# Optimization experiments

Measured on AMD Instinct MI355X. Metric: run time of the kernel, lower is better.

## Reference

```python
import jax, jax.numpy as jnp
import numpy as np

N = 10000
E = 80000
NUM_TYPES = 1000
IN_CH = 64
EMB = 128
IN_GNN = EMB + IN_CH - 1  # 191
NUM_GRAPHS = 16
NUM_CLASSES = 2


def _glorot(key, shape):
    fan_in, fan_out = shape[0], shape[1]
    lim = jnp.sqrt(6.0 / (fan_in + fan_out))
    return jax.random.uniform(key, shape, jnp.float32, -lim, lim)


def setup_inputs() -> dict:
    key = jax.random.key(0)
    ks = jax.random.split(key, 20)
    node_type_ids = jax.random.randint(ks[0], (N,), 0, NUM_TYPES)
    other_feats = jax.random.normal(ks[1], (N, IN_CH - 1), jnp.float32)
    edge_index = jax.random.randint(ks[2], (2, E), 0, N)
    batch = jnp.sort(jax.random.randint(ks[3], (N,), 0, NUM_GRAPHS))
    params = dict(
        emb=jax.random.normal(ks[4], (NUM_TYPES, EMB), jnp.float32),
        W1=_glorot(ks[5], (IN_GNN, 2048)), b1=jnp.zeros((2048,), jnp.float32),
        W2=_glorot(ks[6], (2048, 1024)), b2=jnp.zeros((1024,), jnp.float32),
        W3=_glorot(ks[7], (1024, 1024)), b3=jnp.zeros((1024,), jnp.float32),
        h1w=_glorot(ks[8], (1024, 1024)), h1b=jnp.zeros((1024,), jnp.float32),
        h2w=_glorot(ks[9], (1024, 1024)), h2b=jnp.zeros((1024,), jnp.float32),
        h3w=_glorot(ks[10], (1024, 512)), h3b=jnp.zeros((512,), jnp.float32),
        ow=_glorot(ks[11], (512, NUM_CLASSES)), ob=jnp.zeros((NUM_CLASSES,), jnp.float32),
    )
    return dict(node_type_ids=node_type_ids, other_feats=other_feats,
                edge_index=edge_index, batch=batch, **params)


def _gcn_norm(edge_index, num_nodes):
    # add self loops + symmetric normalization D^-1/2 (A+I) D^-1/2 (PyG GCNConv defaults)
    loop = jnp.arange(num_nodes, dtype=edge_index.dtype)
    src = jnp.concatenate([edge_index[0], loop])
    dst = jnp.concatenate([edge_index[1], loop])
    deg = jax.ops.segment_sum(jnp.ones_like(src, jnp.float32), dst, num_segments=num_nodes)
    dinv = jnp.where(deg > 0, jax.lax.rsqrt(jnp.maximum(deg, 1.0)), 0.0)
    norm = dinv[src] * dinv[dst]
    return src, dst, norm


def _gcn_conv(x, src, dst, norm, W, b):
    h = x @ W                                    # [N, out] dense GEMM first (PyG order)
    msg = h[src] * norm[:, None]                 # gather + scale over edges
    agg = jax.ops.segment_sum(msg, dst, num_segments=x.shape[0])  # scatter-add
    return agg + b


def reference(node_type_ids, other_feats, edge_index, batch,
              emb, W1, b1, W2, b2, W3, b3,
              h1w, h1b, h2w, h2b, h3w, h3b, ow, ob):
    # eval mode: dropout is identity
    x = jnp.concatenate([emb[node_type_ids], other_feats], axis=-1)  # [N, 191]
    src, dst, norm = _gcn_norm(edge_index, x.shape[0])
    x = jax.nn.relu(_gcn_conv(x, src, dst, norm, W1, b1))
    x = jax.nn.relu(_gcn_conv(x, src, dst, norm, W2, b2))
    x = jax.nn.relu(_gcn_conv(x, src, dst, norm, W3, b3))
    # global mean pool over graphs
    sums = jax.ops.segment_sum(x, batch, num_segments=NUM_GRAPHS)
    cnts = jax.ops.segment_sum(jnp.ones((x.shape[0],), jnp.float32), batch, num_segments=NUM_GRAPHS)
    g = sums / jnp.maximum(cnts, 1.0)[:, None]   # [G, 1024]
    g = jax.nn.relu(g @ h1w + h1b)
    g = jax.nn.relu(g @ h2w + h2b)
    g = jax.nn.relu(g @ h3w + h3b)
    return g @ ow + ob                           # [G, num_classes]
```

## Files before the change

### kernel.cpp

```cpp
#include <hip/hip_runtime.h>


#define N_NODES 10000
#define N_EDGES 80000
#define EMB_DIM 128
#define FEAT_DIM 63
#define IN_GNN 191
#define IN_STRIDE 192
#define H1 2048
#define H2 1024
#define NGRAPH 16
#define NCLS 2
#define PCHUNK 8

using ushort = unsigned short;
typedef __attribute__((ext_vector_type(8))) short s8b;
typedef __attribute__((ext_vector_type(4))) float f4v;

__device__ __forceinline__ float us2f(ushort u) {
    union { unsigned int i; float f; } v; v.i = ((unsigned int)u) << 16; return v.f;
}
__device__ __forceinline__ ushort f2us(float f) {
    union { unsigned int i; float f; } v; v.f = f;
    unsigned int r = v.i + 0x7FFFu + ((v.i >> 16) & 1u);
    return (ushort)(r >> 16);
}
__device__ __forceinline__ float ldm(const void* p, long i, int md) {
    return (md == 1) ? us2f(((const ushort*)p)[i]) : ((const float*)p)[i];
}

__global__ void GraphV1EmbLarge_73864847556672_kernel() {}

__global__ void k_detect(const ushort* __restrict__ feats, int* __restrict__ mode) {
    if (threadIdx.x != 0 || blockIdx.x != 0) return;
    int sane = 0;
    for (int i = 0; i < 256; i++) {
        ushort u = feats[i];
        int e = (u >> 7) & 0xFF;
        if (u == 0 || (e >= 97 && e <= 157)) sane++;
    }
    *mode = (sane >= 220) ? 1 : 2;
}

__global__ void k_zero2(int* __restrict__ a, int na, float* __restrict__ b, int nb) {
    int i = blockIdx.x * 256 + threadIdx.x;
    if (i < na) a[i] = 0;
    if (i < nb) b[i] = 0.f;
}
__global__ void k_deg_i(const int* __restrict__ dst, int* __restrict__ cnt) {
    int e = blockIdx.x * blockDim.x + threadIdx.x;
    if (e < N_EDGES) atomicAdd(&cnt[dst[e]], 1);
}
__global__ void k_scan(const int* __restrict__ cnt, int* __restrict__ indptr,
                       float* __restrict__ dinv) {
    __shared__ int part[256];
    int t = threadIdx.x;
    int base = t * 40;
    int s = 0;
    for (int i = 0; i < 40; i++) { int idx = base + i; if (idx < N_NODES) s += cnt[idx]; }
    part[t] = s;
    __syncthreads();
    if (t == 0) {
        int run = 0;
        for (int i = 0; i < 256; i++) { int tmp = part[i]; part[i] = run; run += tmp; }
        indptr[N_NODES] = run;
    }
    __syncthreads();
    int run = part[t];
    for (int i = 0; i < 40; i++) {
        int idx = base + i;
        if (idx < N_NODES) {
            indptr[idx] = run; run += cnt[idx];
            dinv[idx] = rsqrtf((float)cnt[idx] + 1.0f);
        }
    }
}
__global__ void k_fill(const int* __restrict__ src, const int* __restrict__ dst,
                       const int* __restrict__ indptr, int* __restrict__ cursor,
                       const float* __restrict__ dinv, int* __restrict__ ecol,
                       float* __restrict__ ewgt) {
    int e = blockIdx.x * blockDim.x + threadIdx.x;
    if (e >= N_EDGES) return;
    int d = dst[e], s = src[e];
    int slot = indptr[d] + atomicAdd(&cursor[d], 1);
    ecol[slot] = s;
    ewgt[slot] = dinv[s] * dinv[d];
}
__global__ void k_starts(const int* __restrict__ batch, int* __restrict__ starts) {
    int i = blockIdx.x * blockDim.x + threadIdx.x;
    if (i > N_NODES) return;
    int bc = (i < N_NODES) ? batch[i] : NGRAPH;
    int bp = (i == 0) ? -1 : batch[i - 1];
    for (int g = bp + 1; g <= bc; g++) starts[g] = i;
}

__global__ void k_build_x0(const int* __restrict__ types, const void* __restrict__ emb,
                           const void* __restrict__ feats, ushort* __restrict__ x0,
                           const int* __restrict__ mode) {
    int md = *mode;
    int i = blockIdx.x;
    int c = threadIdx.x;
    float v = 0.f;
    if (c < EMB_DIM) v = ldm(emb, (long)types[i] * EMB_DIM + c, md);
    else if (c < IN_GNN) v = ldm(feats, (long)i * FEAT_DIM + (c - EMB_DIM), md);
    x0[(long)i * IN_STRIDE + c] = f2us(v);
}

__device__ __forceinline__ void cvt_tile(const void* W, int K, int N, int Kp,
                                         ushort* Wt, int n0, int k0, int md) {
    __shared__ float tile[32][33];
    int tx = threadIdx.x, ty = threadIdx.y;
    for (int r = ty; r < 32; r += 8) {
        int k = k0 + r;
        tile[r][tx] = (k < K) ? ldm(W, (long)k * N + n0 + tx, md) : 0.f;
    }
    __syncthreads();
    for (int r = ty; r < 32; r += 8) {
        int nn = n0 + r, kk = k0 + tx;
        if (kk < Kp) Wt[(long)nn * Kp + kk] = f2us(tile[tx][r]);
    }
}

__global__ void k_cvtT_all(const void* W1, const void* W2, const void* W3,
                           const void* h1, const void* h2, const void* h3,
                           ushort* W1t, ushort* W2t, ushort* W3t,
                           ushort* h1t, ushort* h2t, ushort* h3t,
                           const int* __restrict__ mode) {
    int md = *mode;
    int b = blockIdx.x;
    if (b < 384) {
        int t = b;        cvt_tile(W1, IN_GNN, H1, IN_STRIDE, W1t, (t % 64) * 32, (t / 64) * 32, md);
    } else if (b < 2432) {
        int t = b - 384;  cvt_tile(W2, H1, H2, H1, W2t, (t % 32) * 32, (t / 32) * 32, md);
    } else if (b < 3456) {
        int t = b - 2432; cvt_tile(W3, H2, H2, H2, W3t, (t % 32) * 32, (t / 32) * 32, md);
    } else if (b < 4480) {
        int t = b - 3456; cvt_tile(h1, H2, H2, H2, h1t, (t % 32) * 32, (t / 32) * 32, md);
    } else if (b < 5504) {
        int t = b - 4480; cvt_tile(h2, H2, H2, H2, h2t, (t % 32) * 32, (t / 32) * 32, md);
    } else {
        int t = b - 5504; cvt_tile(h3, H2, 512, H2, h3t, (t % 16) * 32, (t / 16) * 32, md);
    }
}

__global__ void k_biases(const void* __restrict__ b1, const void* __restrict__ b2,
                         const void* __restrict__ b3, float* __restrict__ b1f,
                         float* __restrict__ b2f, float* __restrict__ b3f,
                         const int* __restrict__ mode) {
    int md = *mode;
    int i = blockIdx.x * 256 + threadIdx.x;
    if (i < 2048) b1f[i] = ldm(b1, i, md);
    else if (i < 3072) b2f[i - 2048] = ldm(b2, (long)(i - 2048), md);
    else if (i < 4096) b3f[i - 3072] = ldm(b3, (long)(i - 3072), md);
}

__global__ void k_gather192(const ushort* __restrict__ H, const int* __restrict__ indptr,
                            const int* __restrict__ ecol, const float* __restrict__ ewgt,
                            const float* __restrict__ dinv, ushort* __restrict__ X) {
    int d = blockIdx.x;
    int c = threadIdx.x;
    float ds = dinv[d];
    float acc = us2f(H[(long)d * IN_STRIDE + c]) * ds * ds;
    int s0 = indptr[d], s1 = indptr[d + 1];
    for (int s = s0; s < s1; s++) {
        int sc = ecol[s];
        float w = ewgt[s];
        acc += us2f(H[(long)sc * IN_STRIDE + c]) * w;
    }
    X[(long)d * IN_STRIDE + c] = f2us(acc);
}

__device__ __forceinline__ void unpack8(uint4 u, float* f) {
    f[0] = us2f((ushort)(u.x & 0xffff)); f[1] = us2f((ushort)(u.x >> 16));
    f[2] = us2f((ushort)(u.y & 0xffff)); f[3] = us2f((ushort)(u.y >> 16));
    f[4] = us2f((ushort)(u.z & 0xffff)); f[5] = us2f((ushort)(u.z >> 16));
    f[6] = us2f((ushort)(u.w & 0xffff)); f[7] = us2f((ushort)(u.w >> 16));
}

__global__ void k_gather1024(const ushort* __restrict__ H, const int* __restrict__ indptr,
                             const int* __restrict__ ecol, const float* __restrict__ ewgt,
                             const float* __restrict__ dinv, const float* __restrict__ bias,
                             ushort* __restrict__ X) {
    int d = blockIdx.x;
    int c8 = threadIdx.x * 8;
    float ds = dinv[d];
    float a[8], f[8];
    unpack8(*(const uint4*)&H[(long)d * H2 + c8], a);
    float w0 = ds * ds;
#pragma unroll
    for (int r = 0; r < 8; r++) a[r] *= w0;
    int s0 = indptr[d], s1 = indptr[d + 1];
    for (int s = s0; s < s1; s++) {
        int sc = ecol[s];
        float w = ewgt[s];
        unpack8(*(const uint4*)&H[(long)sc * H2 + c8], f);
#pragma unroll
        for (int r = 0; r < 8; r++) a[r] += f[r] * w;
    }
    uint4 o;
    unsigned int p0 = (unsigned int)f2us(fmaxf(a[0] + bias[c8 + 0], 0.f));
    unsigned int p1 = (unsigned int)f2us(fmaxf(a[1] + bias[c8 + 1], 0.f));
    unsigned int p2 = (unsigned int)f2us(fmaxf(a[2] + bias[c8 + 2], 0.f));
    unsigned int p3 = (unsigned int)f2us(fmaxf(a[3] + bias[c8 + 3], 0.f));
    unsigned int p4 = (unsigned int)f2us(fmaxf(a[4] + bias[c8 + 4], 0.f));
    unsigned int p5 = (unsigned int)f2us(fmaxf(a[5] + bias[c8 + 5], 0.f));
    unsigned int p6 = (unsigned int)f2us(fmaxf(a[6] + bias[c8 + 6], 0.f));
    unsigned int p7 = (unsigned int)f2us(fmaxf(a[7] + bias[c8 + 7], 0.f));
    o.x = p0 | (p1 << 16); o.y = p2 | (p3 << 16);
    o.z = p4 | (p5 << 16); o.w = p6 | (p7 << 16);
    *(uint4*)&X[(long)d * H2 + c8] = o;
}

__global__ __launch_bounds__(256) void k_mfma_gemm(
    const ushort* __restrict__ A, int lda, int M,
    const ushort* __restrict__ Wt, int K, int N,
    const float* __restrict__ bias, int relu,
    ushort* __restrict__ C, int NB) {
    __shared__ ushort As[128 * 32];
    __shared__ ushort Bs[128 * 32];
    int L = blockIdx.x;
    int i = L >> 3;
    int m_t = (L & 7) + (i / NB) * 8;
    int n_t = i % NB;
    int m0 = m_t * 128, n0 = n_t * 128;
    if (m0 >= M) return;
    int tid = threadIdx.x;
    int wave = tid >> 6, lane = tid & 63;
    int wm = (wave & 1) * 64, wn = (wave >> 1) * 64;
    int quad = lane >> 4, l16 = lane & 15;
    int srow = tid >> 2;
    int scol = (tid & 3) * 8;
    int swz = ((srow >> 1) & 3) << 3;
    int rwz = ((l16 >> 1) & 3) << 3;
    int wa0 = srow * 32 + (scol ^ swz);
    int wa1 = (64 + srow) * 32 + (scol ^ swz);

    f4v acc[4][4];
#pragma unroll
    for (int ii = 0; ii < 4; ii++)
#pragma unroll
        for (int jj = 0; jj < 4; jj++) acc[ii][jj] = (f4v)(0.f);

    int gm1 = m0 + srow;       if (gm1 >= M) gm1 = M - 1;
    int gm2 = m0 + 64 + srow;  if (gm2 >= M) gm2 = M - 1;
    const ushort* pa1 = A + (long)gm1 * lda + scol;
    const ushort* pa2 = A + (long)gm2 * lda + scol;
    const ushort* pb1 = Wt + (long)(n0 + srow) * K + scol;
    const ushort* pb2 = Wt + (long)(n0 + 64 + srow) * K + scol;

    s8b va1 = *(const s8b*)pa1;
    s8b va2 = *(const s8b*)pa2;
    s8b vb1 = *(const s8b*)pb1;
    s8b vb2 = *(const s8b*)pb2;

    for (int k0 = 0; k0 < K; k0 += 32) {
        __syncthreads();
        *(s8b*)&As[wa0] = va1;
        *(s8b*)&As[wa1] = va2;
        *(s8b*)&Bs[wa0] = vb1;
        *(s8b*)&Bs[wa1] = vb2;
        __syncthreads();
        if (k0 + 32 < K) {
            pa1 += 32; pa2 += 32; pb1 += 32; pb2 += 32;
            va1 = *(const s8b*)pa1;
            va2 = *(const s8b*)pa2;
            vb1 = *(const s8b*)pb1;
            vb2 = *(const s8b*)pb2;
        }
        s8b a[4], b[4];
#pragma unroll
        for (int ii = 0; ii < 4; ii++)
            a[ii] = *(const s8b*)&As[(wm + ii * 16 + l16) * 32 + (quad * 8 ^ rwz)];
#pragma unroll
        for (int jj = 0; jj < 4; jj++)
            b[jj] = *(const s8b*)&Bs[(wn + jj * 16 + l16) * 32 + (quad * 8 ^ rwz)];
#pragma unroll
        for (int ii = 0; ii < 4; ii++)
#pragma unroll
            for (int jj = 0; jj < 4; jj++)
                acc[ii][jj] = __builtin_amdgcn_mfma_f32_16x16x32_bf16(a[ii], b[jj], acc[ii][jj], 0, 0, 0);
    }

#pragma unroll
    for (int ii = 0; ii < 4; ii++) {
        int row0 = m0 + wm + ii * 16 + quad * 4;
#pragma unroll
        for (int jj = 0; jj < 4; jj++) {
            int colc = n0 + wn + jj * 16 + l16;
            float bv = bias ? bias[colc] : 0.f;
#pragma unroll
            for (int r = 0; r < 4; r++) {
                int row = row0 + r;
                if (row < M) {
                    float v = acc[ii][jj][r] + bv;
                    if (relu) v = fmaxf(v, 0.f);
                    C[(long)row * N + colc] = f2us(v);
                }
            }
        }
    }
}

__global__ void k_pool_part(const ushort* __restrict__ x, const int* __restrict__ starts,
                            float* __restrict__ acc) {
    int g = blockIdx.x / PCHUNK, ch = blockIdx.x % PCHUNK;
    int c = blockIdx.y * 256 + threadIdx.x;
    int s0 = starts[g], s1 = starts[g + 1];
    int len = s1 - s0;
    int per = (len + PCHUNK - 1) / PCHUNK;
    int r0 = s0 + ch * per;
    int r1 = r0 + per; if (r1 > s1) r1 = s1;
    if (r0 >= r1) return;
    float sum = 0.f;
    for (int i = r0; i < r1; i++) sum += us2f(x[(long)i * H2 + c]);
    atomicAdd(&acc[g * H2 + c], sum);
}
__global__ void k_pool_fin(const float* __restrict__ acc, const int* __restrict__ starts,
                           ushort* __restrict__ pA) {
    int idx = blockIdx.x * 256 + threadIdx.x;
    if (idx >= NGRAPH * H2) return;
    int g = idx >> 10;
    int cnt = starts[g + 1] - starts[g];
    pA[idx] = f2us(acc[idx] / (float)(cnt > 0 ? cnt : 1));
}

__global__ __launch_bounds__(256) void k_head_mfma(const ushort* __restrict__ A,
                                                   const ushort* __restrict__ Wt,
                                                   float* __restrict__ pt, int N) {
    __shared__ float red[4][16][16];
    int n0 = blockIdx.x * 16;
    int ks = blockIdx.y;
    int wave = threadIdx.x >> 6, lane = threadIdx.x & 63;
    int l16 = lane & 15, quad = lane >> 4;
    int kbase = ks * 256 + wave * 64;
    f4v acc = (f4v)(0.f);
#pragma unroll
    for (int kk = 0; kk < 64; kk += 32) {
        int k = kbase + kk + quad * 8;
        s8b a = *(const s8b*)&A[l16 * 1024 + k];
        s8b b = *(const s8b*)&Wt[(long)(n0 + l16) * 1024 + k];
        acc = __builtin_amdgcn_mfma_f32_16x16x32_bf16(a, b, acc, 0, 0, 0);
    }
#pragma unroll
    for (int r = 0; r < 4; r++) red[wave][quad * 4 + r][l16] = acc[r];
    __syncthreads();
    int row = threadIdx.x >> 4, col = threadIdx.x & 15;
    float s = red[0][row][col] + red[1][row][col] + red[2][row][col] + red[3][row][col];
    pt[((long)ks * 16 + row) * N + n0 + col] = s;
}

__global__ void k_head_red(const float* __restrict__ pt, const void* __restrict__ bias,
                           ushort* __restrict__ out, int N,
                           const int* __restrict__ mode) {
    int md = *mode;
    int idx = blockIdx.x * 256 + threadIdx.x;
    if (idx >= 16 * N) return;
    int row = idx / N, col = idx - row * N;
    float s = pt[((long)0 * 16 + row) * N + col] + pt[((long)1 * 16 + row) * N + col]
            + pt[((long)2 * 16 + row) * N + col] + pt[((long)3 * 16 + row) * N + col];
    s = fmaxf(s + ldm(bias, (long)col, md), 0.f);
    out[(long)row * N + col] = f2us(s);
}

__global__ void k_head_out(const ushort* __restrict__ in, const void* __restrict__ W,
                           const void* __restrict__ b, void* __restrict__ out,
                           const int* __restrict__ mode) {
    int md = *mode;
    int row = blockIdx.x >> 1, cls = blockIdx.x & 1;
    int lane = threadIdx.x;
    float acc = 0.f;
    for (int k = lane; k < 512; k += 64)
        acc += us2f(in[row * 512 + k]) * ldm(W, (long)k * NCLS + cls, md);
#pragma unroll
    for (int off = 32; off > 0; off >>= 1) acc += __shfl_down(acc, off);
    if (lane == 0) {
        float v = acc + ldm(b, (long)cls, md);
        if (md == 1) ((ushort*)out)[row * NCLS + cls] = f2us(v);
        else ((float*)out)[row * NCLS + cls] = v;
    }
}

extern "C" void kernel_launch(void* const* d_in, const int* in_sizes, int n_in,
                              void* d_out, int out_size, void* d_ws, size_t ws_size,
                              hipStream_t stream) {
    static const int EXPECT[19] = {
        10000, 630000, 160000, 10000, 128000,
        391168, 2048, 2097152, 1024, 1048576, 1024,
        1048576, 1024, 1048576, 1024, 524288, 512, 1024, 2
    };
    if (n_in != 19) { hipMemsetAsync(d_out, 0x48, 64, stream); return; }
    for (int i = 0; i < 19; i++)
        if (in_sizes[i] != EXPECT[i]) { hipMemsetAsync(d_out, 0x50 + i, 64, stream); return; }
    if (ws_size < (size_t)90000000) { hipMemsetAsync(d_out, 0x49, 64, stream); return; }

    const int* node_types = (const int*)d_in[0];
    const void* other = d_in[1];
    const int* e_src = (const int*)d_in[2];
    const int* e_dst = e_src + N_EDGES;
    const int* batch = (const int*)d_in[3];

    char* w = (char*)d_ws;
    int* mode = (int*)w;      w += 256;
    int* cnt = (int*)w;       w += 10240 * 4;
    int* cursor = (int*)w;    w += 10240 * 4;
    float* dinv = (float*)w;  w += 10240 * 4;
    int* starts = (int*)w;    w += 256;
    int* indptr = (int*)w;    w += 10240 * 4;
    int* ecol = (int*)w;      w += 81920 * 4;
    float* ewgt = (float*)w;  w += 81920 * 4;
    float* b1f = (float*)w;   w += 2048 * 4;
    float* b2f = (float*)w;   w += 1024 * 4;
    float* b3f = (float*)w;   w += 1024 * 4;
    float* pt = (float*)w;    w += 4 * 16 * 1024 * 4;
    float* pacc = (float*)w;  w += 16 * 1024 * 4;
    ushort* pA = (ushort*)w;  w += 16 * 1024 * 2;
    ushort* hA = (ushort*)w;  w += 16 * 1024 * 2;
    ushort* hB = (ushort*)w;  w += 16 * 1024 * 2;
    ushort* x0 = (ushort*)w;  w += 1920000 * 2;
    ushort* A1 = (ushort*)w;  w += 1920000 * 2;
    ushort* W1t = (ushort*)w; w += 393216 * 2;
    ushort* W2t = (ushort*)w; w += 2097152 * 2;
    ushort* W3t = (ushort*)w; w += 1048576 * 2;
    ushort* h1wt = (ushort*)w; w += 1048576 * 2;
    ushort* h2wt = (ushort*)w; w += 1048576 * 2;
    ushort* h3wt = (ushort*)w; w += 524288 * 2;
    ushort* Hb = (ushort*)w;  w += 20480000 * 2;
    ushort* Gb = (ushort*)w;  w += 10240000 * 2;
    ushort* x2 = Hb;
    ushort* x3 = Hb + (size_t)N_NODES * H2;

    hipGetLastError();
    k_detect<<<1, 64, 0, stream>>>((const ushort*)other, mode);
    hipError_t e0 = hipGetLastError();
    if (e0 != hipSuccess) { hipMemsetAsync(d_out, 0x46, 64, stream); return; }

    k_zero2<<<80, 256, 0, stream>>>(cnt, 20480, pacc, NGRAPH * H2);
    k_deg_i<<<(N_EDGES + 255) / 256, 256, 0, stream>>>(e_dst, cnt);
    k_starts<<<(N_NODES + 256) / 256, 256, 0, stream>>>(batch, starts);
    k_scan<<<1, 256, 0, stream>>>(cnt, indptr, dinv);
    k_fill<<<(N_EDGES + 255) / 256, 256, 0, stream>>>(e_src, e_dst, indptr, cursor, dinv, ecol, ewgt);

    k_build_x0<<<N_NODES, IN_STRIDE, 0, stream>>>(node_types, d_in[4], other, x0, mode);
    k_cvtT_all<<<6016, dim3(32, 8), 0, stream>>>(d_in[5], d_in[7], d_in[9], d_in[11], d_in[13], d_in[15],
                                                 W1t, W2t, W3t, h1wt, h2wt, h3wt, mode);
    k_biases<<<16, 256, 0, stream>>>(d_in[6], d_in[8], d_in[10], b1f, b2f, b3f, mode);

    k_gather192<<<N_NODES, IN_STRIDE, 0, stream>>>(x0, indptr, ecol, ewgt, dinv, A1);
    k_mfma_gemm<<<16 * 80, 256, 0, stream>>>(A1, IN_STRIDE, N_NODES, W1t, IN_STRIDE, H1, b1f, 1, Hb, 16);

    k_mfma_gemm<<<8 * 80, 256, 0, stream>>>(Hb, H1, N_NODES, W2t, H1, H2, nullptr, 0, Gb, 8);
    k_gather1024<<<N_NODES, 128, 0, stream>>>(Gb, indptr, ecol, ewgt, dinv, b2f, x2);

    k_mfma_gemm<<<8 * 80, 256, 0, stream>>>(x2, H2, N_NODES, W3t, H2, H2, nullptr, 0, Gb, 8);
    k_gather1024<<<N_NODES, 128, 0, stream>>>(Gb, indptr, ecol, ewgt, dinv, b3f, x3);

    k_pool_part<<<dim3(NGRAPH * PCHUNK, H2 / 256), 256, 0, stream>>>(x3, starts, pacc);
    k_pool_fin<<<64, 256, 0, stream>>>(pacc, starts, pA);

    k_head_mfma<<<dim3(64, 4), 256, 0, stream>>>(pA, h1wt, pt, 1024);
    k_head_red<<<64, 256, 0, stream>>>(pt, d_in[12], hA, 1024, mode);
    k_head_mfma<<<dim3(64, 4), 256, 0, stream>>>(hA, h2wt, pt, 1024);
    k_head_red<<<64, 256, 0, stream>>>(pt, d_in[14], hB, 1024, mode);
    k_head_mfma<<<dim3(32, 4), 256, 0, stream>>>(hB, h3wt, pt, 512);
    k_head_red<<<32, 256, 0, stream>>>(pt, d_in[16], hA, 512, mode);
    k_head_out<<<NGRAPH * NCLS, 64, 0, stream>>>(hA, d_in[17], d_in[18], d_out, mode);

    hipError_t e1 = hipGetLastError();
    if (e1 != hipSuccess) hipMemsetAsync(d_out, 0x47, 64, stream);
}
```

Baseline: 408.9 us.

## Double-buffer GEMM shared tiles and unroll sparse gather loops by two

The bf16 MFMA GEMM now uses two LDS buffers for the A and B tiles. The next K-slice is written into the alternate buffer while the current one is consumed, which drops one __syncthreads per K iteration. Separately, both CSR gather kernels process two neighbor edges per loop iteration so two row loads are in flight together, raising memory-level parallelism. The cost is doubled LDS use in the GEMM, which may reduce occupancy, plus slightly higher register pressure in the gathers.

After: 403.1 us. Within noise of the previous version (-1.4%).

```diff
diff --git a/kernel.cpp b/kernel.cpp
--- a/kernel.cpp
+++ b/kernel.cpp
@@ -162,11 +162,15 @@
     float ds = dinv[d];
     float acc = us2f(H[(long)d * IN_STRIDE + c]) * ds * ds;
     int s0 = indptr[d], s1 = indptr[d + 1];
-    for (int s = s0; s < s1; s++) {
-        int sc = ecol[s];
-        float w = ewgt[s];
-        acc += us2f(H[(long)sc * IN_STRIDE + c]) * w;
-    }
+    int s = s0;
+    for (; s + 1 < s1; s += 2) {
+        int sa = ecol[s], sb = ecol[s + 1];
+        float wa = ewgt[s], wb = ewgt[s + 1];
+        float fa = us2f(H[(long)sa * IN_STRIDE + c]);
+        float fb = us2f(H[(long)sb * IN_STRIDE + c]);
+        acc += fa * wa + fb * wb;
+    }
+    if (s < s1) acc += us2f(H[(long)ecol[s] * IN_STRIDE + c]) * ewgt[s];
     X[(long)d * IN_STRIDE + c] = f2us(acc);
 }
 
@@ -184,18 +188,29 @@
     int d = blockIdx.x;
     int c8 = threadIdx.x * 8;
     float ds = dinv[d];
-    float a[8], f[8];
+    float a[8], f0[8], f1[8];
     unpack8(*(const uint4*)&H[(long)d * H2 + c8], a);
     float w0 = ds * ds;
 #pragma unroll
     for (int r = 0; r < 8; r++) a[r] *= w0;
     int s0 = indptr[d], s1 = indptr[d + 1];
-    for (int s = s0; s < s1; s++) {
-        int sc = ecol[s];
-        float w = ewgt[s];
-        unpack8(*(const uint4*)&H[(long)sc * H2 + c8], f);
-#pragma unroll
-        for (int r = 0; r < 8; r++) a[r] += f[r] * w;
+    int s = s0;
+    for (; s + 1 < s1; s += 2) {
+        int sa = ecol[s], sb = ecol[s + 1];
+        float wa = ewgt[s], wb = ewgt[s + 1];
+        uint4 ua = *(const uint4*)&H[(long)sa * H2 + c8];
+        uint4 ub = *(const uint4*)&H[(long)sb * H2 + c8];
+        unpack8(ua, f0);
+        unpack8(ub, f1);
+#pragma unroll
+        for (int r = 0; r < 8; r++) a[r] += f0[r] * wa + f1[r] * wb;
+    }
+    if (s < s1) {
+        uint4 ua = *(const uint4*)&H[(long)ecol[s] * H2 + c8];
+        float wa = ewgt[s];
+        unpack8(ua, f0);
+#pragma unroll
+        for (int r = 0; r < 8; r++) a[r] += f0[r] * wa;
     }
     uint4 o;
     unsigned int p0 = (unsigned int)f2us(fmaxf(a[0] + bias[c8 + 0], 0.f));
@@ -216,8 +231,8 @@
     const ushort* __restrict__ Wt, int K, int N,
     const float* __restrict__ bias, int relu,
     ushort* __restrict__ C, int NB) {
-    __shared__ ushort As[128 * 32];
-    __shared__ ushort Bs[128 * 32];
+    __shared__ ushort As[2][128 * 32];
+    __shared__ ushort Bs[2][128 * 32];
     int L = blockIdx.x;
     int i = L >> 3;
     int m_t = (L & 7) + (i / NB) * 8;
@@ -248,32 +263,47 @@
     const ushort* pb1 = Wt + (long)(n0 + srow) * K + scol;
     const ushort* pb2 = Wt + (long)(n0 + 64 + srow) * K + scol;
 
+    int niter = K >> 5;
     s8b va1 = *(const s8b*)pa1;
     s8b va2 = *(const s8b*)pa2;
     s8b vb1 = *(const s8b*)pb1;
     s8b vb2 = *(const s8b*)pb2;
-
-    for (int k0 = 0; k0 < K; k0 += 32) {
+    *(s8b*)&As[0][wa0] = va1;
+    *(s8b*)&As[0][wa1] = va2;
+    *(s8b*)&Bs[0][wa0] = vb1;
+    *(s8b*)&Bs[0][wa1] = vb2;
+    if (niter > 1) {
+        pa1 += 32; pa2 += 32; pb1 += 32; pb2 += 32;
+        va1 = *(const s8b*)pa1;
+        va2 = *(const s8b*)pa2;
+        vb1 = *(const s8b*)pb1;
+        vb2 = *(const s8b*)pb2;
+    }
+
+    for (int it = 0; it < niter; it++) {
+        int cur = it & 1;
         __syncthreads();
-        *(s8b*)&As[wa0] = va1;
-        *(s8b*)&As[wa1] = va2;
-        *(s8b*)&Bs[wa0] = vb1;
-        *(s8b*)&Bs[wa1] = vb2;
-        __syncthreads();
-        if (k0 + 32 < K) {
-            pa1 += 32; pa2 += 32; pb1 += 32; pb2 += 32;
-            va1 = *(const s8b*)pa1;
-            va2 = *(const s8b*)pa2;
-            vb1 = *(const s8b*)pb1;
-            vb2 = *(const s8b*)pb2;
+        if (it + 1 < niter) {
+            int nxt = cur ^ 1;
+            *(s8b*)&As[nxt][wa0] = va1;
+            *(s8b*)&As[nxt][wa1] = va2;
+            *(s8b*)&Bs[nxt][wa0] = vb1;
+            *(s8b*)&Bs[nxt][wa1] = vb2;
+            if (it + 2 < niter) {
+                pa1 += 32; pa2 += 32; pb1 += 32; pb2 += 32;
+                va1 = *(const s8b*)pa1;
+                va2 = *(const s8b*)pa2;
+                vb1 = *(const s8b*)pb1;
+                vb2 = *(const s8b*)pb2;
+            }
         }
         s8b a[4], b[4];
 #pragma unroll
         for (int ii = 0; ii < 4; ii++)
-            a[ii] = *(const s8b*)&As[(wm + ii * 16 + l16) * 32 + (quad * 8 ^ rwz)];
+            a[ii] = *(const s8b*)&As[cur][(wm + ii * 16 + l16) * 32 + (quad * 8 ^ rwz)];
 #pragma unroll
         for (int jj = 0; jj < 4; jj++)
-            b[jj] = *(const s8b*)&Bs[(wn + jj * 16 + l16) * 32 + (quad * 8 ^ rwz)];
+            b[jj] = *(const s8b*)&Bs[cur][(wn + jj * 16 + l16) * 32 + (quad * 8 ^ rwz)];
 #pragma unroll
         for (int ii = 0; ii < 4; ii++)
 #pragma unroll
```
